# Kernel tuning notes

Measured on AMD Instinct MI355X. Metric: run time of the kernel, lower is better.

Reference implementation:

```python
import jax, jax.numpy as jnp
import numpy as np

NUM_CLS = 80
NUM_CONVS = 4
GROUPS = 32
STRIDES = [8, 16, 32, 64, 128]
SIZES = [32.0, 64.0, 128.0, 256.0, 512.0]
CLS_BIAS_INIT = -float(np.log((1 - 0.01) / 0.01))


def _conv(x, w, b):
    # NCHW 3x3 stride-1 same-pad conv
    y = jax.lax.conv_general_dilated(x, w, (1, 1), 'SAME',
                                     dimension_numbers=('NCHW', 'OIHW', 'NCHW'))
    return y + b[None, :, None, None]


def _group_norm(x, gamma, beta, eps=1e-5):
    B, C, H, W = x.shape
    xr = x.reshape(B, GROUPS, C // GROUPS, H, W)
    m = xr.mean(axis=(2, 3, 4), keepdims=True)
    v = xr.var(axis=(2, 3, 4), keepdims=True)
    xn = ((xr - m) / jnp.sqrt(v + eps)).reshape(B, C, H, W)
    return xn * gamma[None, :, None, None] + beta[None, :, None, None]


def _tower(x, ws, bs, gs, betas):
    # CGR block: Conv -> GroupNorm -> ReLU, repeated NUM_CONVS times
    for i in range(NUM_CONVS):
        x = jax.nn.relu(_group_norm(_conv(x, ws[i], bs[i]), gs[i], betas[i]))
    return x


def _build_anchors(h, w, stride, size):
    half = size / 2.0  # single scale=1, ratio=1 -> one square anchor per cell
    yv, xv = jnp.meshgrid(jnp.arange(h, dtype=jnp.float32),
                          jnp.arange(w, dtype=jnp.float32), indexing='ij')
    grid = jnp.stack([xv, yv, xv, yv], axis=-1)  # [h,w,4]
    delta = jnp.array([-half, -half, half, half], dtype=jnp.float32)
    return ((grid + 0.5) * stride + delta).reshape(-1, 4)  # [h*w,4]


def setup_inputs() -> dict:
    key = jax.random.key(0)
    ks = jax.random.split(key, 16)
    C = 256
    feats = {}
    hw = [80, 40, 20, 10, 5]
    for i, name in enumerate(['p3', 'p4', 'p5', 'p6', 'p7']):
        feats[name] = jax.random.normal(ks[i], (8, C, hw[i], hw[i]), dtype=jnp.float32)
    std = 0.01
    inp = dict(feats)
    # cls tower
    inp['cls_tw'] = jax.random.normal(ks[5], (NUM_CONVS, C, C, 3, 3), jnp.float32) * std
    inp['cls_tb'] = jnp.zeros((NUM_CONVS, C), jnp.float32)
    inp['cls_tg'] = jnp.ones((NUM_CONVS, C), jnp.float32)
    inp['cls_tbeta'] = jnp.zeros((NUM_CONVS, C), jnp.float32)
    # reg tower
    inp['reg_tw'] = jax.random.normal(ks[6], (NUM_CONVS, C, C, 3, 3), jnp.float32) * std
    inp['reg_tb'] = jnp.zeros((NUM_CONVS, C), jnp.float32)
    inp['reg_tg'] = jnp.ones((NUM_CONVS, C), jnp.float32)
    inp['reg_tbeta'] = jnp.zeros((NUM_CONVS, C), jnp.float32)
    # heads (num_anchors = 1)
    inp['cls_hw'] = jax.random.normal(ks[7], (NUM_CLS, C, 3, 3), jnp.float32) * std
    inp['cls_hb'] = jnp.full((NUM_CLS,), CLS_BIAS_INIT, jnp.float32)
    inp['reg_hw'] = jax.random.normal(ks[8], (4, C, 3, 3), jnp.float32) * std
    inp['reg_hb'] = jnp.zeros((4,), jnp.float32)
    inp['iou_hw'] = jax.random.normal(ks[9], (1, C, 3, 3), jnp.float32) * std
    inp['iou_hb'] = jnp.zeros((1,), jnp.float32)
    inp['scales'] = jnp.ones((5,), jnp.float32)
    return inp


def reference(p3, p4, p5, p6, p7,
              cls_tw, cls_tb, cls_tg, cls_tbeta,
              reg_tw, reg_tb, reg_tg, reg_tbeta,
              cls_hw, cls_hb, reg_hw, reg_hb, iou_hw, iou_hb, scales):
    feats = [p3, p4, p5, p6, p7]
    outs = []
    for j, x in enumerate(feats):
        B, _, H, W = x.shape
        ct = _tower(x, cls_tw, cls_tb, cls_tg, cls_tbeta)
        rt = _tower(x, reg_tw, reg_tb, reg_tg, reg_tbeta)
        # heads: permute to NHWC then flatten spatial (num_anchors=1)
        cls = _conv(ct, cls_hw, cls_hb).transpose(0, 2, 3, 1).reshape(B, -1, NUM_CLS)
        reg = _conv(rt, reg_hw, reg_hb).transpose(0, 2, 3, 1).reshape(B, -1, 4) * scales[j]
        iou = _conv(rt, iou_hw, iou_hb).transpose(0, 2, 3, 1).reshape(B, -1, 1)  # on_reg=True
        # decode boxes against anchors
        anchor = _build_anchors(H, W, STRIDES[j], SIZES[j])  # [HW,4]
        awh = anchor[:, 2:] - anchor[:, :2]
        actr = anchor[:, :2] + 0.5 * awh
        xy = reg[..., :2] * awh + actr
        wh = jnp.exp(reg[..., 2:]) * awh
        box = jnp.concatenate([xy - 0.5 * wh, xy + 0.5 * wh], axis=-1)
        outs.append(jnp.concatenate([box, iou, cls], axis=-1))
    return jnp.concatenate(outs, axis=1)  # [B, 8525, 85]
```

## Files before the change

### kernel.cpp

```cpp
#include <hip/hip_runtime.h>
#include <stdint.h>

typedef unsigned short u16;
typedef unsigned int u32;
typedef short short8 __attribute__((ext_vector_type(8)));
typedef float f32x4 __attribute__((ext_vector_type(4)));

struct LevelTab {
  int Hf[5], Wf[5], Hp[5], Wp[5], HW[5], M[5], mtcum[5], aoff[5];
  long xoffp[5], moff[5], ppcum[5], mcum[5];
  float asize[5], astride[5];
};

__device__ __forceinline__ u16 f2bf(float f) {
  u32 u = __float_as_uint(f);
  u = (u + 0x7fffu + ((u >> 16) & 1u)) >> 16;
  return (u16)u;
}
__device__ __forceinline__ float bflo(u32 v) { return __uint_as_float(v << 16); }
__device__ __forceinline__ float bfhi(u32 v) { return __uint_as_float(v & 0xffff0000u); }

__device__ __forceinline__ void gload16(const void* g, void* l) {
  __builtin_amdgcn_global_load_lds((__attribute__((address_space(1))) void*)(g),
                                   (__attribute__((address_space(3))) void*)(l),
                                   16, 0, 0);
}

__global__ __launch_bounds__(256) void prep_tower_w(const float* __restrict__ cls_tw,
                                                    const float* __restrict__ reg_tw,
                                                    u16* __restrict__ W2t) {
  long t = (long)blockIdx.x * 256 + threadIdx.x;
  const long total = 2L * 4 * 256 * 2304;
  if (t >= total) return;
  int ci = (int)(t & 255);
  long u = t >> 8;
  int j = (int)(u % 9); u /= 9;
  int co = (int)(u & 255); u >>= 8;
  int layer = (int)(u & 3);
  int tw = (int)(u >> 2);
  const float* src = tw ? reg_tw : cls_tw;
  float v = src[(((long)layer * 256 + co) * 256 + ci) * 9 + j];
  W2t[t] = f2bf(v);
}

__global__ __launch_bounds__(256) void prep_cls_w(const float* __restrict__ cls_hw,
                                                  u16* __restrict__ W2c) {
  long t = (long)blockIdx.x * 256 + threadIdx.x;
  if (t >= 128L * 2304) return;
  int ci = (int)(t & 255);
  long u = t >> 8;
  int j = (int)(u % 9);
  int co = (int)(u / 9);
  float v = (co < 80) ? cls_hw[(((long)co * 256 + ci) * 9 + j)] : 0.f;
  W2c[t] = f2bf(v);
}

__global__ __launch_bounds__(256) void prep_reg_w(const float* __restrict__ reg_hw,
                                                  const float* __restrict__ iou_hw,
                                                  u16* __restrict__ W2r) {
  long t = (long)blockIdx.x * 256 + threadIdx.x;
  if (t >= 5L * 2304) return;
  int ci = (int)(t & 255);
  long u = t >> 8;
  int j = (int)(u % 9);
  int o = (int)(u / 9);
  float v = (o < 4) ? reg_hw[(((long)o * 256 + ci) * 9 + j)] : iou_hw[(long)ci * 9 + j];
  W2r[t] = f2bf(v);
}

__global__ __launch_bounds__(256) void convert_in(const float* __restrict__ i0, const float* __restrict__ i1,
                                                  const float* __restrict__ i2, const float* __restrict__ i3,
                                                  const float* __restrict__ i4, u16* __restrict__ X0,
                                                  LevelTab lt) {
  long t = (long)blockIdx.x * 256 + threadIdx.x;
  if (t >= lt.ppcum[4] * 32) return;
  const int c8 = (int)(t & 31);
  long pp = t >> 5;
  int lvl = 0;
#pragma unroll
  for (int i = 0; i < 4; ++i) lvl += (pp >= lt.ppcum[i]);
  const long lp = pp - (lvl ? lt.ppcum[lvl - 1] : 0);
  const int Hp = lt.Hp[lvl], Wp = lt.Wp[lvl], Wf = lt.Wf[lvl], HW = lt.HW[lvl];
  const int HpWp = Hp * Wp;
  const int n = (int)(lp / HpWp);
  const int rem = (int)(lp - (long)n * HpWp);
  const int yp = rem / Wp, xp = rem - yp * Wp;
  u16* op = X0 + (lt.xoffp[lvl] + lp) * 256 + c8 * 8;
  if (yp == 0 || yp == Hp - 1 || xp == 0 || xp == Wp - 1) {
    *(uint4*)op = make_uint4(0u, 0u, 0u, 0u);
    return;
  }
  const float* src = lvl == 0 ? i0 : lvl == 1 ? i1 : lvl == 2 ? i2 : lvl == 3 ? i3 : i4;
  const int y = yp - 1, x = xp - 1;
  const long sb = ((long)n * 256 + c8 * 8) * HW + (long)y * Wf + x;
  u32 o4[4];
#pragma unroll
  for (int i = 0; i < 4; ++i) {
    float f0 = src[sb + (long)(2 * i) * HW];
    float f1 = src[sb + (long)(2 * i + 1) * HW];
    o4[i] = (u32)f2bf(f0) | ((u32)f2bf(f1) << 16);
  }
  *(uint4*)op = make_uint4(o4[0], o4[1], o4[2], o4[3]);
}

template <int MODE>
__global__ __launch_bounds__(256, 2) void conv_mfma(const u16* __restrict__ Xpad,
                                                    const u16* __restrict__ W2,
                                                    const float* __restrict__ bias,
                                                    u16* __restrict__ Otmp,
                                                    float* __restrict__ Oout, LevelTab lt) {
  __shared__ __align__(16) u16 sA[3][128 * 32];
  __shared__ __align__(16) u16 sB[3][128 * 32];

  const int nwg = gridDim.x;
  const int qq = nwg >> 3, rr = nwg & 7;
  const int xcd = blockIdx.x & 7, ib = blockIdx.x >> 3;
  const int sid = (xcd < rr ? xcd * (qq + 1) : rr * (qq + 1) + (xcd - rr) * qq) + ib;
  const int tileId = (MODE == 0) ? (sid >> 1) : sid;
  const int nt = (MODE == 0) ? (sid & 1) : 0;

  int lvl = 0;
#pragma unroll
  for (int i = 0; i < 4; ++i) lvl += (tileId >= lt.mtcum[i]);
  const int mt = tileId - (lvl ? lt.mtcum[lvl - 1] : 0);
  const int Hp = lt.Hp[lvl], Wp = lt.Wp[lvl], Wf = lt.Wf[lvl];
  const int HW = lt.HW[lvl], M = lt.M[lvl];
  const long xbase = lt.xoffp[lvl] * 256;

  const int tid = threadIdx.x;
  const int w = tid >> 6, lane = tid & 63;
  const int rsub = lane >> 2;
  const int r0 = w * 16 + rsub;
  const int q2 = ((lane & 3) - ((lane >> 3) & 3)) & 3;

  long gA[2], gB[2];
#pragma unroll
  for (int i = 0; i < 2; ++i) {
    int ml = mt * 128 + r0 + i * 64;
    if (ml > M - 1) ml = M - 1;
    const int n = ml / HW;
    const int pr = ml - n * HW;
    const int y = pr / Wf;
    const int x = pr - y * Wf;
    gA[i] = xbase + ((long)((n * Hp + y) * Wp + x)) * 256 + q2 * 8;
    gB[i] = (long)(nt * 128 + r0 + i * 64) * 2304 + q2 * 8;
  }

  const int wm = w >> 1, wn = w & 1;
  const int lm = lane & 15;
  const int slot8 = ((((lane >> 4) + ((lane >> 1) & 3)) & 3) << 3);

  f32x4 acc[4][4];
#pragma unroll
  for (int a = 0; a < 4; ++a)
#pragma unroll
    for (int c = 0; c < 4; ++c) acc[a][c] = {0.f, 0.f, 0.f, 0.f};

  auto STAGE = [&](int kk, int buf) {
    const int j = kk >> 3;
    const int c0 = (kk & 7) << 5;
    const int jy = j / 3, jx = j - jy * 3;
    const long aK = ((long)(jy * Wp + jx)) * 256 + c0;
    const long bK = (long)kk << 5;
    gload16(Xpad + gA[0] + aK, sA[buf] + w * 512);
    gload16(Xpad + gA[1] + aK, sA[buf] + 2048 + w * 512);
    gload16(W2 + gB[0] + bK, sB[buf] + w * 512);
    gload16(W2 + gB[1] + bK, sB[buf] + 2048 + w * 512);
  };

  short8 a0[4], b0[4], a1[4], b1[4];
  auto FRAG0 = [&](int cur) {
    const u16* pa = sA[cur];
    const u16* pb = sB[cur];
#pragma unroll
    for (int mi = 0; mi < 4; ++mi)
      a0[mi] = *(const short8*)(pa + ((wm * 64 + mi * 16 + lm) << 5) + slot8);
#pragma unroll
    for (int ni = 0; ni < 4; ++ni)
      b0[ni] = *(const short8*)(pb + ((wn * 64 + ni * 16 + lm) << 5) + slot8);
  };
  auto FRAG1 = [&](int cur) {
    const u16* pa = sA[cur];
    const u16* pb = sB[cur];
#pragma unroll
    for (int mi = 0; mi < 4; ++mi)
      a1[mi] = *(const short8*)(pa + ((wm * 64 + mi * 16 + lm) << 5) + slot8);
#pragma unroll
    for (int ni = 0; ni < 4; ++ni)
      b1[ni] = *(const short8*)(pb + ((wn * 64 + ni * 16 + lm) << 5) + slot8);
  };
  auto MFMA0 = [&]() {
    __builtin_amdgcn_s_setprio(1);
#pragma unroll
    for (int mi = 0; mi < 4; ++mi)
#pragma unroll
      for (int ni = 0; ni < 4; ++ni)
        acc[mi][ni] = __builtin_amdgcn_mfma_f32_16x16x32_bf16(a0[mi], b0[ni], acc[mi][ni], 0, 0, 0);
    __builtin_amdgcn_s_setprio(0);
  };
  auto MFMA1 = [&]() {
    __builtin_amdgcn_s_setprio(1);
#pragma unroll
    for (int mi = 0; mi < 4; ++mi)
#pragma unroll
      for (int ni = 0; ni < 4; ++ni)
        acc[mi][ni] = __builtin_amdgcn_mfma_f32_16x16x32_bf16(a1[mi], b1[ni], acc[mi][ni], 0, 0, 0);
    __builtin_amdgcn_s_setprio(0);
  };

  STAGE(0, 0);
  STAGE(1, 1);
  asm volatile("s_waitcnt vmcnt(4)" ::: "memory");
  __builtin_amdgcn_s_barrier();
  FRAG0(0);
  STAGE(2, 2);

  int rd = 1;
  int st = 0;
  for (int kk = 0; kk < 68; kk += 2) {
    asm volatile("s_waitcnt vmcnt(4)" ::: "memory");
    __builtin_amdgcn_s_barrier();
    FRAG1(rd);
    rd = rd == 2 ? 0 : rd + 1;
    STAGE(kk + 3, st);
    st = st == 2 ? 0 : st + 1;
    MFMA0();
    asm volatile("s_waitcnt vmcnt(4)" ::: "memory");
    __builtin_amdgcn_s_barrier();
    FRAG0(rd);
    rd = rd == 2 ? 0 : rd + 1;
    STAGE(kk + 4, st);
    st = st == 2 ? 0 : st + 1;
    MFMA1();
  }
  asm volatile("s_waitcnt vmcnt(4)" ::: "memory");
  __builtin_amdgcn_s_barrier();
  FRAG1(rd);
  rd = rd == 2 ? 0 : rd + 1;
  STAGE(71, st);
  MFMA0();
  asm volatile("s_waitcnt vmcnt(4)" ::: "memory");
  __builtin_amdgcn_s_barrier();
  FRAG0(rd);
  rd = rd == 2 ? 0 : rd + 1;
  MFMA1();
  asm volatile("s_waitcnt vmcnt(0)" ::: "memory");
  __builtin_amdgcn_s_barrier();
  FRAG1(rd);
  MFMA0();
  MFMA1();

  const int mwb = mt * 128 + wm * 64;
  const int colb = nt * 128 + wn * 64;
  const int rq4 = (lane >> 4) << 2;
#pragma unroll
  for (int ni = 0; ni < 4; ++ni) {
    const int col = colb + ni * 16 + lm;
    if (MODE == 1 && col >= 80) continue;
    const float bv = bias[col];
#pragma unroll
    for (int mi = 0; mi < 4; ++mi) {
      const int rb = mwb + mi * 16 + rq4;
#pragma unroll
      for (int rg = 0; rg < 4; ++rg) {
        const int ml = rb + rg;
        if (ml < M) {
          const float v = acc[mi][ni][rg] + bv;
          if (MODE == 0) {
            Otmp[(lt.moff[lvl] + ml) * 256 + col] = f2bf(v);
          } else {
            const int nb = ml / HW;
            const int pr = ml - nb * HW;
            Oout[((long)nb * 8525 + lt.aoff[lvl] + pr) * 85 + 5 + col] = v;
          }
        }
      }
    }
  }
}

__global__ __launch_bounds__(256) void gn_stats(const u16* __restrict__ tmp,
                                                float* __restrict__ stats, LevelTab lt) {
  const int bid = blockIdx.x;
  const int lvl = bid >> 8, bg = bid & 255, b = bg >> 5, g = bg & 31;
  const int HW = lt.HW[lvl];
  const long base = (lt.moff[lvl] + (long)b * HW) * 256 + g * 8;
  float s = 0.f, ss = 0.f;
  for (int p = threadIdx.x; p < HW; p += 256) {
    const uint4 r = *(const uint4*)(tmp + base + (long)p * 256);
    const u32 u[4] = {r.x, r.y, r.z, r.w};
#pragma unroll
    for (int i = 0; i < 4; ++i) {
      float f0 = bflo(u[i]), f1 = bfhi(u[i]);
      s += f0 + f1;
      ss += f0 * f0 + f1 * f1;
    }
  }
#pragma unroll
  for (int o = 32; o; o >>= 1) {
    s += __shfl_down(s, o);
    ss += __shfl_down(ss, o);
  }
  __shared__ float rs[4], rss[4];
  const int w = threadIdx.x >> 6, lane = threadIdx.x & 63;
  if (lane == 0) { rs[w] = s; rss[w] = ss; }
  __syncthreads();
  if (threadIdx.x == 0) {
    s = rs[0] + rs[1] + rs[2] + rs[3];
    ss = rss[0] + rss[1] + rss[2] + rss[3];
    const float inv = 1.f / (float)(HW * 8);
    const float mean = s * inv;
    const float var = ss * inv - mean * mean;
    stats[bid * 2 + 0] = mean;
    stats[bid * 2 + 1] = rsqrtf(var + 1e-5f);
  }
}

__global__ __launch_bounds__(256) void gn_apply(const u16* __restrict__ tmp,
                                                const float* __restrict__ stats,
                                                const float* __restrict__ gamma,
                                                const float* __restrict__ beta,
                                                u16* __restrict__ pout, LevelTab lt) {
  long t = (long)blockIdx.x * 256 + threadIdx.x;
  if (t >= lt.ppcum[4] * 32) return;
  const int c8 = (int)(t & 31);
  long pp = t >> 5;
  int lvl = 0;
#pragma unroll
  for (int i = 0; i < 4; ++i) lvl += (pp >= lt.ppcum[i]);
  const long lp = pp - (lvl ? lt.ppcum[lvl - 1] : 0);
  const int Hp = lt.Hp[lvl], Wp = lt.Wp[lvl], Wf = lt.Wf[lvl], HW = lt.HW[lvl];
  const int HpWp = Hp * Wp;
  const int n = (int)(lp / HpWp);
  const int rem = (int)(lp - (long)n * HpWp);
  const int yp = rem / Wp, xp = rem - yp * Wp;
  u16* op = pout + (lt.xoffp[lvl] + lp) * 256 + c8 * 8;
  if (yp == 0 || yp == Hp - 1 || xp == 0 || xp == Wp - 1) {
    *(uint4*)op = make_uint4(0u, 0u, 0u, 0u);
    return;
  }
  const long m = lt.moff[lvl] + (long)n * HW + (long)(yp - 1) * Wf + (xp - 1);
  const uint4 r = *(const uint4*)(tmp + m * 256 + c8 * 8);
  const int sidx = (lvl * 256 + n * 32 + c8) * 2;
  const float mean = stats[sidx], rstd = stats[sidx + 1];
  const u32 u[4] = {r.x, r.y, r.z, r.w};
  u32 o4[4];
#pragma unroll
  for (int i = 0; i < 4; ++i) {
    const int c = c8 * 8 + i * 2;
    float f0 = (bflo(u[i]) - mean) * rstd * gamma[c] + beta[c];
    float f1 = (bfhi(u[i]) - mean) * rstd * gamma[c + 1] + beta[c + 1];
    f0 = fmaxf(f0, 0.f);
    f1 = fmaxf(f1, 0.f);
    o4[i] = (u32)f2bf(f0) | ((u32)f2bf(f1) << 16);
  }
  *(uint4*)op = make_uint4(o4[0], o4[1], o4[2], o4[3]);
}

__global__ __launch_bounds__(256) void regiou_decode(const u16* __restrict__ Xp,
                                                     const u16* __restrict__ W2r,
                                                     const float* __restrict__ reg_hb,
                                                     const float* __restrict__ iou_hb,
                                                     const float* __restrict__ scales,
                                                     float* __restrict__ out, LevelTab lt) {
  const long gt = (long)blockIdx.x * 256 + threadIdx.x;
  const int gw = (int)(gt >> 6);
  const int lane = threadIdx.x & 63;
  if (gw >= (int)lt.mcum[4]) return;
  int lvl = 0;
#pragma unroll
  for (int i = 0; i < 4; ++i) lvl += (gw >= (int)lt.mcum[i]);
  const int m = gw - (int)(lvl ? lt.mcum[lvl - 1] : 0);
  const int HW = lt.HW[lvl], Wf = lt.Wf[lvl], Hp = lt.Hp[lvl], Wp = lt.Wp[lvl];
  const int b = m / HW, pr = m - b * HW;
  const int y = pr / Wf, x = pr - y * Wf;
  const long base = (lt.xoffp[lvl] + (long)(b * Hp + y) * Wp + x) * 256 + lane * 4;
  float acc[5] = {0.f, 0.f, 0.f, 0.f, 0.f};
#pragma unroll
  for (int j = 0; j < 9; ++j) {
    const int jy = j / 3, jx = j - jy * 3;
    const uint2 ar = *(const uint2*)(Xp + base + ((long)(jy * Wp + jx)) * 256);
    const float x0 = bflo(ar.x), x1 = bfhi(ar.x), x2 = bflo(ar.y), x3 = bfhi(ar.y);
#pragma unroll
    for (int o = 0; o < 5; ++o) {
      const uint2 wr = *(const uint2*)(W2r + o * 2304 + j * 256 + lane * 4);
      acc[o] += x0 * bflo(wr.x) + x1 * bfhi(wr.x) + x2 * bflo(wr.y) + x3 * bfhi(wr.y);
    }
  }
#pragma unroll
  for (int o = 0; o < 5; ++o)
#pragma unroll
    for (int d = 32; d; d >>= 1) acc[o] += __shfl_down(acc[o], d);
  if (lane == 0) {
    const float sc = scales[lvl];
    const float r0 = (acc[0] + reg_hb[0]) * sc;
    const float r1 = (acc[1] + reg_hb[1]) * sc;
    const float r2 = (acc[2] + reg_hb[2]) * sc;
    const float r3 = (acc[3] + reg_hb[3]) * sc;
    const float iou = acc[4] + iou_hb[0];
    const float st = lt.astride[lvl], sz = lt.asize[lvl];
    const float cx = (x + 0.5f) * st, cy = (y + 0.5f) * st;
    const float xx = r0 * sz + cx, yy = r1 * sz + cy;
    const float ww = expf(r2) * sz, hh = expf(r3) * sz;
    float* o = out + ((long)b * 8525 + lt.aoff[lvl] + pr) * 85;
    o[0] = xx - 0.5f * ww;
    o[1] = yy - 0.5f * hh;
    o[2] = xx + 0.5f * ww;
    o[3] = yy + 0.5f * hh;
    o[4] = iou;
  }
}

extern "C" void kernel_launch(void* const* d_in, const int* in_sizes, int n_in, void* d_out,
                              int out_size, void* d_ws, size_t ws_size, hipStream_t stream) {
  const float* feats[5];
  for (int i = 0; i < 5; ++i) feats[i] = (const float*)d_in[i];
  const float* cls_tw = (const float*)d_in[5];
  const float* cls_tb = (const float*)d_in[6];
  const float* cls_tg = (const float*)d_in[7];
  const float* cls_tbeta = (const float*)d_in[8];
  const float* reg_tw = (const float*)d_in[9];
  const float* reg_tb = (const float*)d_in[10];
  const float* reg_tg = (const float*)d_in[11];
  const float* reg_tbeta = (const float*)d_in[12];
  const float* cls_hw = (const float*)d_in[13];
  const float* cls_hb = (const float*)d_in[14];
  const float* reg_hw = (const float*)d_in[15];
  const float* reg_hb = (const float*)d_in[16];
  const float* iou_hw = (const float*)d_in[17];
  const float* iou_hb = (const float*)d_in[18];
  const float* scales = (const float*)d_in[19];
  float* out = (float*)d_out;

  LevelTab lt;
  const int Hs[5] = {80, 40, 20, 10, 5};
  const float sizes[5] = {32.f, 64.f, 128.f, 256.f, 512.f};
  const float strides[5] = {8.f, 16.f, 32.f, 64.f, 128.f};
  long ppc = 0, mc = 0;
  int mtc = 0, ao = 0;
  for (int i = 0; i < 5; ++i) {
    const int H = Hs[i];
    lt.Hf[i] = H; lt.Wf[i] = H; lt.Hp[i] = H + 2; lt.Wp[i] = H + 2;
    lt.HW[i] = H * H; lt.M[i] = 8 * H * H;
    lt.xoffp[i] = ppc; lt.moff[i] = mc; lt.aoff[i] = ao;
    ppc += 8L * (H + 2) * (H + 2);
    mc += lt.M[i];
    mtc += (lt.M[i] + 127) / 128;
    lt.ppcum[i] = ppc; lt.mcum[i] = mc; lt.mtcum[i] = mtc;
    ao += H * H;
    lt.asize[i] = sizes[i]; lt.astride[i] = strides[i];
  }

  char* ws = (char*)d_ws;
  size_t off = 0;
  auto take = [&](size_t bytes) {
    off = (off + 255) & ~(size_t)255;
    char* p = ws + off;
    off += bytes;
    return p;
  };
  u16* X0 = (u16*)take((size_t)ppc * 256 * 2);
  u16* padA = (u16*)take((size_t)ppc * 256 * 2);
  u16* padB = (u16*)take((size_t)ppc * 256 * 2);
  u16* tmp = (u16*)take((size_t)mc * 256 * 2);
  u16* W2t = (u16*)take((size_t)2 * 4 * 256 * 2304 * 2);
  u16* W2c = (u16*)take((size_t)128 * 2304 * 2);
  u16* W2r = (u16*)take((size_t)5 * 2304 * 2);
  float* stats = (float*)take((size_t)5 * 256 * 2 * 4);

  prep_tower_w<<<(int)((2L * 4 * 256 * 2304 + 255) / 256), 256, 0, stream>>>(cls_tw, reg_tw, W2t);
  prep_cls_w<<<(int)((128L * 2304 + 255) / 256), 256, 0, stream>>>(cls_hw, W2c);
  prep_reg_w<<<(int)((5L * 2304 + 255) / 256), 256, 0, stream>>>(reg_hw, iou_hw, W2r);

  const int ppBlocks = (int)((ppc * 32 + 255) / 256);
  convert_in<<<ppBlocks, 256, 0, stream>>>(feats[0], feats[1], feats[2], feats[3], feats[4], X0, lt);

  u16* pads[2] = {padA, padB};
  for (int tw = 0; tw < 2; ++tw) {
    const float* tb = tw ? reg_tb : cls_tb;
    const float* tg = tw ? reg_tg : cls_tg;
    const float* tbe = tw ? reg_tbeta : cls_tbeta;
    const u16* cur = X0;
    for (int layer = 0; layer < 4; ++layer) {
      const u16* w2 = W2t + (size_t)(tw * 4 + layer) * 256 * 2304;
      conv_mfma<0><<<mtc * 2, 256, 0, stream>>>(cur, w2, tb + layer * 256, tmp, nullptr, lt);
      gn_stats<<<5 * 256, 256, 0, stream>>>(tmp, stats, lt);
      u16* nxt = pads[layer & 1];
      gn_apply<<<ppBlocks, 256, 0, stream>>>(tmp, stats, tg + layer * 256, tbe + layer * 256, nxt, lt);
      cur = nxt;
    }
    if (tw == 0) {
      conv_mfma<1><<<mtc, 256, 0, stream>>>(cur, W2c, cls_hb, nullptr, out, lt);
    } else {
      regiou_decode<<<(int)((mc * 64 + 255) / 256), 256, 0, stream>>>(cur, W2r, reg_hb, iou_hb,
                                                                      scales, out, lt);
    }
  }
}
```

Baseline: 1.562 ms.

## Batch cls and reg tower layers into shared conv and GroupNorm launches

The conv, GroupNorm-stats and GroupNorm-apply kernels now each take two sets of pointers and split their grid by a path index, so the cls and reg towers run layer by layer in the same launches. This halves the number of tower launches and doubles the grid per launch, which is meant to reduce launch overhead and partial-wave tail effects on the smaller pyramid levels. It needs two extra activation buffers and a second scratch buffer, so a fallback keeps the old sequential schedule when the workspace is too small. The extra pointer selection adds a few scalar instructions per block.

New measurement: 1.522 ms. 1.03x faster.

```diff
diff --git a/kernel.cpp b/kernel.cpp
--- a/kernel.cpp
+++ b/kernel.cpp
@@ -104,11 +104,12 @@
 }
 
 template <int MODE>
-__global__ __launch_bounds__(256, 2) void conv_mfma(const u16* __restrict__ Xpad,
-                                                    const u16* __restrict__ W2,
-                                                    const float* __restrict__ bias,
-                                                    u16* __restrict__ Otmp,
-                                                    float* __restrict__ Oout, LevelTab lt) {
+__global__ __launch_bounds__(256, 2) void conv_mfma(
+    const u16* __restrict__ XpadA, const u16* __restrict__ XpadB,
+    const u16* __restrict__ W2A, const u16* __restrict__ W2B,
+    const float* __restrict__ biasA, const float* __restrict__ biasB,
+    u16* __restrict__ OtmpA, u16* __restrict__ OtmpB,
+    float* __restrict__ Oout, int NP, LevelTab lt) {
   __shared__ __align__(16) u16 sA[3][128 * 32];
   __shared__ __align__(16) u16 sB[3][128 * 32];
 
@@ -116,8 +117,22 @@
   const int qq = nwg >> 3, rr = nwg & 7;
   const int xcd = blockIdx.x & 7, ib = blockIdx.x >> 3;
   const int sid = (xcd < rr ? xcd * (qq + 1) : rr * (qq + 1) + (xcd - rr) * qq) + ib;
-  const int tileId = (MODE == 0) ? (sid >> 1) : sid;
-  const int nt = (MODE == 0) ? (sid & 1) : 0;
+
+  int path, tileId, nt;
+  if (MODE == 0) {
+    const int tn = (NP == 2) ? (sid >> 1) : sid;
+    path = (NP == 2) ? (sid & 1) : 0;
+    tileId = tn >> 1;
+    nt = tn & 1;
+  } else {
+    path = 0;
+    tileId = sid;
+    nt = 0;
+  }
+  const u16* __restrict__ Xpad = path ? XpadB : XpadA;
+  const u16* __restrict__ W2 = path ? W2B : W2A;
+  const float* __restrict__ bias = path ? biasB : biasA;
+  u16* __restrict__ Otmp = path ? OtmpB : OtmpA;
 
   int lvl = 0;
 #pragma unroll
@@ -279,10 +294,14 @@
   }
 }
 
-__global__ __launch_bounds__(256) void gn_stats(const u16* __restrict__ tmp,
+__global__ __launch_bounds__(256) void gn_stats(const u16* __restrict__ tmpA,
+                                                const u16* __restrict__ tmpB,
                                                 float* __restrict__ stats, LevelTab lt) {
   const int bid = blockIdx.x;
-  const int lvl = bid >> 8, bg = bid & 255, b = bg >> 5, g = bg & 31;
+  const int path = bid / 1280;
+  const int lb = bid - path * 1280;
+  const u16* __restrict__ tmp = path ? tmpB : tmpA;
+  const int lvl = lb >> 8, bg = lb & 255, b = bg >> 5, g = bg & 31;
   const int HW = lt.HW[lvl];
   const long base = (lt.moff[lvl] + (long)b * HW) * 256 + g * 8;
   float s = 0.f, ss = 0.f;
@@ -316,12 +335,23 @@
   }
 }
 
-__global__ __launch_bounds__(256) void gn_apply(const u16* __restrict__ tmp,
+__global__ __launch_bounds__(256) void gn_apply(const u16* __restrict__ tmpA,
+                                                const u16* __restrict__ tmpB,
                                                 const float* __restrict__ stats,
-                                                const float* __restrict__ gamma,
-                                                const float* __restrict__ beta,
-                                                u16* __restrict__ pout, LevelTab lt) {
-  long t = (long)blockIdx.x * 256 + threadIdx.x;
+                                                const float* __restrict__ gammaA,
+                                                const float* __restrict__ betaA,
+                                                const float* __restrict__ gammaB,
+                                                const float* __restrict__ betaB,
+                                                u16* __restrict__ poutA, u16* __restrict__ poutB,
+                                                int ppBlocks, LevelTab lt) {
+  const int path = blockIdx.x / ppBlocks;
+  const int xb = blockIdx.x - path * ppBlocks;
+  const u16* __restrict__ tmp = path ? tmpB : tmpA;
+  const float* __restrict__ gamma = path ? gammaB : gammaA;
+  const float* __restrict__ beta = path ? betaB : betaA;
+  u16* __restrict__ pout = path ? poutB : poutA;
+
+  long t = (long)xb * 256 + threadIdx.x;
   if (t >= lt.ppcum[4] * 32) return;
   const int c8 = (int)(t & 31);
   long pp = t >> 5;
@@ -341,7 +371,7 @@
   }
   const long m = lt.moff[lvl] + (long)n * HW + (long)(yp - 1) * Wf + (xp - 1);
   const uint4 r = *(const uint4*)(tmp + m * 256 + c8 * 8);
-  const int sidx = (lvl * 256 + n * 32 + c8) * 2;
+  const int sidx = (path * 1280 + lvl * 256 + n * 32 + c8) * 2;
   const float mean = stats[sidx], rstd = stats[sidx + 1];
   const u32 u[4] = {r.x, r.y, r.z, r.w};
   u32 o4[4];
@@ -459,41 +489,96 @@
     off += bytes;
     return p;
   };
-  u16* X0 = (u16*)take((size_t)ppc * 256 * 2);
-  u16* padA = (u16*)take((size_t)ppc * 256 * 2);
-  u16* padB = (u16*)take((size_t)ppc * 256 * 2);
-  u16* tmp = (u16*)take((size_t)mc * 256 * 2);
-  u16* W2t = (u16*)take((size_t)2 * 4 * 256 * 2304 * 2);
-  u16* W2c = (u16*)take((size_t)128 * 2304 * 2);
-  u16* W2r = (u16*)take((size_t)5 * 2304 * 2);
-  float* stats = (float*)take((size_t)5 * 256 * 2 * 4);
-
-  prep_tower_w<<<(int)((2L * 4 * 256 * 2304 + 255) / 256), 256, 0, stream>>>(cls_tw, reg_tw, W2t);
-  prep_cls_w<<<(int)((128L * 2304 + 255) / 256), 256, 0, stream>>>(cls_hw, W2c);
-  prep_reg_w<<<(int)((5L * 2304 + 255) / 256), 256, 0, stream>>>(reg_hw, iou_hw, W2r);
+  auto alg = [](size_t v) { return (v + 255) & ~(size_t)255; };
+  const size_t sizeX = alg((size_t)ppc * 512);
+  const size_t sizeT = alg((size_t)mc * 512);
+  const size_t wTsz = alg((size_t)2 * 4 * 256 * 2304 * 2);
+  const size_t wCsz = alg((size_t)128 * 2304 * 2);
+  const size_t wRsz = alg((size_t)5 * 2304 * 2);
+  const size_t sSsz = alg((size_t)2 * 1280 * 2 * 4);
+  const size_t needMerged = 4 * sizeX + 2 * sizeT + wTsz + wCsz + wRsz + sSsz + 4096;
+  const bool MERGED = (ws_size >= needMerged);
 
   const int ppBlocks = (int)((ppc * 32 + 255) / 256);
-  convert_in<<<ppBlocks, 256, 0, stream>>>(feats[0], feats[1], feats[2], feats[3], feats[4], X0, lt);
-
-  u16* pads[2] = {padA, padB};
-  for (int tw = 0; tw < 2; ++tw) {
-    const float* tb = tw ? reg_tb : cls_tb;
-    const float* tg = tw ? reg_tg : cls_tg;
-    const float* tbe = tw ? reg_tbeta : cls_tbeta;
-    const u16* cur = X0;
+
+  if (MERGED) {
+    u16* X0 = (u16*)take(sizeX);
+    u16* C1 = (u16*)take(sizeX);
+    u16* R0 = (u16*)take(sizeX);
+    u16* R1 = (u16*)take(sizeX);
+    u16* tmpA = (u16*)take(sizeT);
+    u16* tmpB = (u16*)take(sizeT);
+    u16* W2t = (u16*)take(wTsz);
+    u16* W2c = (u16*)take(wCsz);
+    u16* W2r = (u16*)take(wRsz);
+    float* stats = (float*)take(sSsz);
+
+    prep_tower_w<<<(int)((2L * 4 * 256 * 2304 + 255) / 256), 256, 0, stream>>>(cls_tw, reg_tw, W2t);
+    prep_cls_w<<<(int)((128L * 2304 + 255) / 256), 256, 0, stream>>>(cls_hw, W2c);
+    prep_reg_w<<<(int)((5L * 2304 + 255) / 256), 256, 0, stream>>>(reg_hw, iou_hw, W2r);
+    convert_in<<<ppBlocks, 256, 0, stream>>>(feats[0], feats[1], feats[2], feats[3], feats[4], X0, lt);
+
+    u16* wrA[4] = {X0, C1, X0, C1};
+    u16* wrB[4] = {R0, R1, R0, R1};
+    const u16* curA = X0;
+    const u16* curB = X0;
     for (int layer = 0; layer < 4; ++layer) {
-      const u16* w2 = W2t + (size_t)(tw * 4 + layer) * 256 * 2304;
-      conv_mfma<0><<<mtc * 2, 256, 0, stream>>>(cur, w2, tb + layer * 256, tmp, nullptr, lt);
-      gn_stats<<<5 * 256, 256, 0, stream>>>(tmp, stats, lt);
-      u16* nxt = pads[layer & 1];
-      gn_apply<<<ppBlocks, 256, 0, stream>>>(tmp, stats, tg + layer * 256, tbe + layer * 256, nxt, lt);
-      cur = nxt;
+      const u16* w2A = W2t + (size_t)(0 * 4 + layer) * 256 * 2304;
+      const u16* w2B = W2t + (size_t)(1 * 4 + layer) * 256 * 2304;
+      conv_mfma<0><<<mtc * 2 * 2, 256, 0, stream>>>(curA, curB, w2A, w2B,
+                                                    cls_tb + layer * 256, reg_tb + layer * 256,
+                                                    tmpA, tmpB, nullptr, 2, lt);
+      gn_stats<<<2 * 1280, 256, 0, stream>>>(tmpA, tmpB, stats, lt);
+      gn_apply<<<2 * ppBlocks, 256, 0, stream>>>(tmpA, tmpB, stats,
+                                                 cls_tg + layer * 256, cls_tbeta + layer * 256,
+                                                 reg_tg + layer * 256, reg_tbeta + layer * 256,
+                                                 wrA[layer], wrB[layer], ppBlocks, lt);
+      curA = wrA[layer];
+      curB = wrB[layer];
     }
-    if (tw == 0) {
-      conv_mfma<1><<<mtc, 256, 0, stream>>>(cur, W2c, cls_hb, nullptr, out, lt);
-    } else {
-      regiou_decode<<<(int)((mc * 64 + 255) / 256), 256, 0, stream>>>(cur, W2r, reg_hb, iou_hb,
-                                                                      scales, out, lt);
+    conv_mfma<1><<<mtc, 256, 0, stream>>>(curA, curA, W2c, W2c, cls_hb, cls_hb,
+                                          nullptr, nullptr, out, 1, lt);
+    regiou_decode<<<(int)((mc * 64 + 255) / 256), 256, 0, stream>>>(curB, W2r, reg_hb, iou_hb,
+                                                                    scales, out, lt);
+  } else {
+    u16* X0 = (u16*)take(sizeX);
+    u16* padA = (u16*)take(sizeX);
+    u16* padB = (u16*)take(sizeX);
+    u16* tmp = (u16*)take(sizeT);
+    u16* W2t = (u16*)take(wTsz);
+    u16* W2c = (u16*)take(wCsz);
+    u16* W2r = (u16*)take(wRsz);
+    float* stats = (float*)take(sSsz);
+
+    prep_tower_w<<<(int)((2L * 4 * 256 * 2304 + 255) / 256), 256, 0, stream>>>(cls_tw, reg_tw, W2t);
+    prep_cls_w<<<(int)((128L * 2304 + 255) / 256), 256, 0, stream>>>(cls_hw, W2c);
+    prep_reg_w<<<(int)((5L * 2304 + 255) / 256), 256, 0, stream>>>(reg_hw, iou_hw, W2r);
+    convert_in<<<ppBlocks, 256, 0, stream>>>(feats[0], feats[1], feats[2], feats[3], feats[4], X0, lt);
+
+    u16* pads[2] = {padA, padB};
+    for (int tw = 0; tw < 2; ++tw) {
+      const float* tb = tw ? reg_tb : cls_tb;
+      const float* tg = tw ? reg_tg : cls_tg;
+      const float* tbe = tw ? reg_tbeta : cls_tbeta;
+      const u16* cur = X0;
+      for (int layer = 0; layer < 4; ++layer) {
+        const u16* w2 = W2t + (size_t)(tw * 4 + layer) * 256 * 2304;
+        conv_mfma<0><<<mtc * 2, 256, 0, stream>>>(cur, cur, w2, w2, tb + layer * 256,
+                                                  tb + layer * 256, tmp, tmp, nullptr, 1, lt);
+        gn_stats<<<1280, 256, 0, stream>>>(tmp, tmp, stats, lt);
+        u16* nxt = pads[layer & 1];
+        gn_apply<<<ppBlocks, 256, 0, stream>>>(tmp, tmp, stats, tg + layer * 256,
+                                               tbe + layer * 256, tg + layer * 256,
+                                               tbe + layer * 256, nxt, nxt, ppBlocks, lt);
+        cur = nxt;
+      }
+      if (tw == 0) {
+        conv_mfma<1><<<mtc, 256, 0, stream>>>(cur, cur, W2c, W2c, cls_hb, cls_hb,
+                                              nullptr, nullptr, out, 1, lt);
+      } else {
+        regiou_decode<<<(int)((mc * 64 + 255) / 256), 256, 0, stream>>>(cur, W2r, reg_hb, iou_hb,
+                                                                        scales, out, lt);
+      }
     }
   }
 }
```
